# Performance work log

Hardware: AMD Instinct MI355X
Metric: run time of the kernel (lower is better)

The kernel has to match this reference:

```python
import jax, jax.numpy as jnp
import numpy as np

B, T, K, H = 8, 1024, 128, 8
TOP_K = 64
KS = 5  # conv kernel size for Q/K
DN = ('NCH', 'OIH', 'NCH')


def setup_inputs() -> dict:
    key = jax.random.key(0)
    ks = jax.random.split(key, 9)
    s = 0.05
    return {
        'x': jax.random.normal(ks[0], (B, T, K), jnp.float32),
        'Wq': jax.random.normal(ks[1], (K * H, K, KS), jnp.float32) * s,
        'bq': jax.random.normal(ks[2], (K * H,), jnp.float32) * s,
        'Wk': jax.random.normal(ks[3], (K * H, K, KS), jnp.float32) * s,
        'bk': jax.random.normal(ks[4], (K * H,), jnp.float32) * s,
        'Wv': jax.random.normal(ks[5], (K * H, K, 1), jnp.float32) * s,
        'bv': jax.random.normal(ks[6], (K * H,), jnp.float32) * s,
        'Wu': jax.random.normal(ks[7], (K, K * H), jnp.float32) * s,
        'bu': jax.random.normal(ks[8], (K,), jnp.float32) * s,
    }


def _prep(z, b, k, h, t, scale):
    # z: (b, k*h, t) conv output; torch view(b,k,h,t) then transposes -> (b,h,t,k)
    z = z.reshape(b, k, h, t)
    z = jnp.transpose(z, (0, 2, 3, 1)) * scale  # (b, h, t, k)
    # torch: transpose(1,2).contiguous().view(b*h, t, k) -- replicate exactly
    z = jnp.transpose(z, (0, 2, 1, 3)).reshape(b * h, t, k)
    return z


def reference(x, Wq, bq, Wk, bk, Wv, bv, Wu, bu):
    b, t, k = x.shape
    h = H
    xc = jnp.transpose(x, (0, 2, 1))  # (b, k, t)
    # causal left-pad KS-1 for Q/K convs; V is pointwise (kernel 1)
    q = jax.lax.conv_general_dilated(xc, Wq, (1,), [(KS - 1, 0)], dimension_numbers=DN) + bq[None, :, None]
    kk = jax.lax.conv_general_dilated(xc, Wk, (1,), [(KS - 1, 0)], dimension_numbers=DN) + bk[None, :, None]
    v = jax.lax.conv_general_dilated(xc, Wv, (1,), [(0, 0)], dimension_numbers=DN) + bv[None, :, None]
    scale = k ** -0.25
    q = _prep(q, b, k, h, t, scale)
    kk = _prep(kk, b, k, h, t, scale)
    v = _prep(v, b, k, h, t, 1.0)
    w = jnp.einsum('btk,bsk->bts', q, kk)  # (b*h, t, t)
    # top-k sparsification: keep entries >= k-th largest per row, else row min
    largest, _ = jax.lax.top_k(w, TOP_K)
    thresh = jnp.min(largest, axis=-1, keepdims=True)
    row_min = jnp.min(w, axis=-1, keepdims=True)
    w = jnp.where(w >= thresh, w, row_min)
    # causal mask (strict upper triangle -> -inf)
    causal = jnp.triu(jnp.ones((t, t), bool), 1)
    w = jnp.where(causal[None], -jnp.inf, w)
    w = jax.nn.softmax(w, axis=-1)
    out = jnp.einsum('bts,bsk->btk', w, v)  # (b*h, t, k)
    out = out.reshape(b, h, t, k)
    out = jnp.transpose(out, (0, 2, 1, 3)).reshape(b, t, k * h)
    return out @ Wu.T + bu
```

## Files before the change

### kernel.cpp

```cpp
#include <hip/hip_runtime.h>
#include <hip/hip_fp16.h>
#include <cstdint>

using f16 = _Float16;
typedef __attribute__((ext_vector_type(8))) _Float16 f16x8;
typedef __attribute__((ext_vector_type(4))) _Float16 f16x4;
typedef __attribute__((ext_vector_type(4))) float f32x4;

#define MFMA16(a, b, c) __builtin_amdgcn_mfma_f32_16x16x32_f16((a), (b), (c), 0, 0, 0)

__device__ __forceinline__ f16x8 ldfrag(const f16* p) { return *(const f16x8*)p; }

__device__ __forceinline__ void dma16(const f16* g, f16* l) {
  __builtin_amdgcn_global_load_lds(
      (const __attribute__((address_space(1))) void*)g,
      (__attribute__((address_space(3))) void*)l, 16, 0, 0);
}
__device__ __forceinline__ void wait_vm0() {
  asm volatile("s_waitcnt vmcnt(0)" ::: "memory");
}
__device__ __forceinline__ void wait_lgkm0() {
  asm volatile("s_waitcnt lgkmcnt(0)" ::: "memory");
}
__device__ __forceinline__ void wait_vm4() {
  asm volatile("s_waitcnt vmcnt(4)" ::: "memory");
}
__device__ __forceinline__ void wait_vm2() {
  asm volatile("s_waitcnt vmcnt(2)" ::: "memory");
}

static const int64_t NX = 1048576;
static const int64_t NW = 655360;
static const int64_t NV = 131072;

__global__ __launch_bounds__(256) void k0_prep(
    const float* __restrict__ x, const float* __restrict__ Wq,
    const float* __restrict__ Wk, const float* __restrict__ Wv,
    const float* __restrict__ Wu,
    f16* __restrict__ xh, f16* __restrict__ xl,
    f16* __restrict__ Wqh, f16* __restrict__ Wql,
    f16* __restrict__ Wkh, f16* __restrict__ Wkl,
    f16* __restrict__ Wvb, f16* __restrict__ Wub) {
  int64_t i = (int64_t)blockIdx.x * 256 + threadIdx.x;
  if (i < NX) {
    const float v = x[i];
    const f16 h = (f16)v;
    xh[i] = h; xl[i] = (f16)(v - (float)h);
  } else if (i < NX + NW) {
    int64_t d = i - NX;
    int j = (int)(d >> 17);
    int rem = (int)(d & 131071);
    int o = rem >> 7, c = rem & 127;
    const float v = Wq[(int64_t)(o * 128 + c) * 5 + j];
    const f16 h = (f16)v;
    Wqh[d] = h; Wql[d] = (f16)(v - (float)h);
  } else if (i < NX + 2 * NW) {
    int64_t d = i - NX - NW;
    int j = (int)(d >> 17);
    int rem = (int)(d & 131071);
    int o = rem >> 7, c = rem & 127;
    const float v = Wk[(int64_t)(o * 128 + c) * 5 + j];
    const f16 h = (f16)v;
    Wkh[d] = h; Wkl[d] = (f16)(v - (float)h);
  } else if (i < NX + 2 * NW + NV) {
    int64_t d = i - NX - 2 * NW;
    Wvb[d] = (f16)Wv[d];
  } else {
    int64_t d = i - NX - 2 * NW - NV;
    Wub[d] = (f16)Wu[d];
  }
}

#define STAGE_QK(DST, PASS, VALEXPR)                                    \
  {                                                                     \
    __syncthreads();                                                    \
    _Pragma("unroll")                                                   \
    for (int nt = 0; nt < 8; ++nt) {                                    \
      const int o = o0 + nt * 16 + lo;                                  \
      const int kcl = (o >> 3) & 63, hh = o & 7;                        \
      _Pragma("unroll")                                                 \
      for (int rtl = 0; rtl < 2; ++rtl) {                               \
        const int rt = (PASS) * 2 + rtl;                                \
        _Pragma("unroll")                                               \
        for (int r = 0; r < 4; ++r) {                                   \
          const int t2l = (rtl * 16 + quad * 4 + r) * 8 + hh;           \
          lds[t2l * 72 + kcl] = (VALEXPR);                              \
        }                                                               \
      }                                                                 \
    }                                                                   \
    __syncthreads();                                                    \
    _Pragma("unroll")                                                   \
    for (int p = 0; p < 8; ++p) {                                       \
      const int idx = p * 256 + tid;                                    \
      const int a = idx >> 3, c8 = (idx & 7) * 8;                       \
      *(f16x8*)(DST + ((int64_t)m * 1024 + t2b + (PASS) * 256 + a) * 128 + \
                half * 64 + c8) = *(const f16x8*)&lds[a * 72 + c8];     \
    }                                                                   \
  }

__global__ __launch_bounds__(256) void k1_conv(
    const f16* __restrict__ xh, const f16* __restrict__ xl,
    const f16* __restrict__ Wqh, const f16* __restrict__ Wql,
    const f16* __restrict__ Wkh, const f16* __restrict__ Wkl,
    const f16* __restrict__ Wvb,
    const float* __restrict__ bq, const float* __restrict__ bk,
    const float* __restrict__ bv,
    f16* __restrict__ q3h, f16* __restrict__ q3l,
    f16* __restrict__ k3h, f16* __restrict__ k3l,
    f16* __restrict__ v3T) {
  __shared__ f16 shm[36384];
  f16* const wbuf = shm;
  f16* const xbuf = shm + 18432;
  f16* const lds  = shm;
  const int tid = threadIdx.x;
  const int w = tid >> 6, lane = tid & 63;
  const int quad = lane >> 4, lo = lane & 15;
  const int r0 = blockIdx.x * 64;
  const int bb = r0 >> 10;
  const int m  = r0 >> 7;
  const int t2b = (r0 & 127) * 8;
  const int tloc = r0 & 1023;
  const int half = blockIdx.y;
  const int isK = blockIdx.z;
  const int o0 = half * 512 + w * 128;

  const f16* Wh = isK ? Wkh : Wqh;
  const f16* Wl = isK ? Wkl : Wql;
  const float* bias = isK ? bk : bq;

#pragma unroll
  for (int p = 0; p < 9; ++p) {
    const int u = p * 256 + tid;
    if (u < 2176) {
      const int row = u >> 5, tz = (u >> 4) & 1, c8 = (u & 15) * 8;
      int lt = tloc - 4 + row;
      if (lt < 0) lt = 0;
      const f16* src = (tz ? xl : xh) + ((int64_t)(bb * 1024 + lt)) * 128 + c8;
      *(f16x8*)&xbuf[row * 264 + tz * 128 + c8] = *(const f16x8*)src;
    }
  }
  __syncthreads();

  const int64_t wlane = (int64_t)(lane & 15) * 128 + (lane >> 4) * 8;

  if (!isK) {
    f32x4 av[4][8];
#pragma unroll
    for (int rt = 0; rt < 4; ++rt)
#pragma unroll
      for (int i = 0; i < 8; ++i)
#pragma unroll
        for (int r = 0; r < 4; ++r) av[rt][i][r] = 0.f;

#pragma unroll
    for (int g = 0; g < 4; ++g) {
#pragma unroll
      for (int s = 0; s < 2; ++s) {
        const int64_t vsrc = (int64_t)(o0 + (g * 2 + s) * 16) * 128 + wlane;
#pragma unroll
        for (int kk = 0; kk < 4; ++kk)
          dma16(Wvb + vsrc + kk * 32, wbuf + w * 4096 + s * 2048 + kk * 512);
      }
      wait_vm0();
#pragma unroll
      for (int kk = 0; kk < 4; ++kk) {
        f16x8 a[4];
#pragma unroll
        for (int rt = 0; rt < 4; ++rt)
          a[rt] = *(const f16x8*)&xbuf[(rt * 16 + lo + 4) * 264 + kk * 32 +
                                       quad * 8];
#pragma unroll
        for (int s = 0; s < 2; ++s) {
          const f16x8 bv8 = *(const f16x8*)&wbuf[w * 4096 + s * 2048 + kk * 512 +
                                                 quad * 128 + lo * 8];
#pragma unroll
          for (int rt = 0; rt < 4; ++rt)
            av[rt][g * 2 + s] = MFMA16(a[rt], bv8, av[rt][g * 2 + s]);
        }
      }
      wait_lgkm0();
    }
    __syncthreads();
#pragma unroll
    for (int pass = 0; pass < 2; ++pass) {
#pragma unroll
      for (int nt = 0; nt < 8; ++nt) {
        const int o = o0 + nt * 16 + lo;
        const float vbv = bv[o];
        const int kcl = (o >> 3) & 63, hh = o & 7;
#pragma unroll
        for (int rtl = 0; rtl < 2; ++rtl)
#pragma unroll
          for (int r = 0; r < 4; ++r) {
            const int t2l = (rtl * 16 + quad * 4 + r) * 8 + hh;
            lds[kcl * 264 + t2l] = (f16)(av[pass * 2 + rtl][nt][r] + vbv);
          }
      }
      __syncthreads();
#pragma unroll
      for (int p = 0; p < 8; ++p) {
        const int idx = p * 256 + tid;
        const int kcl = idx >> 5, t8 = (idx & 31) * 8;
        *(f16x8*)(v3T + ((int64_t)m * 128 + half * 64 + kcl) * 1024 + t2b +
                  pass * 256 + t8) = *(const f16x8*)&lds[kcl * 264 + t8];
      }
      __syncthreads();
    }
  }

  f32x4 aq[4][8];
#pragma unroll
  for (int rt = 0; rt < 4; ++rt)
#pragma unroll
    for (int i = 0; i < 8; ++i)
#pragma unroll
      for (int r = 0; r < 4; ++r) { aq[rt][i][r] = 0.f; }

  const int64_t wbase = wlane + (int64_t)o0 * 128;
#define ISSUE_HALF(J, KK, NTG, H)                                       \
  {                                                                     \
    _Pragma("unroll")                                                   \
    for (int ntl2 = 0; ntl2 < 2; ++ntl2) {                              \
      const int ntl_ = (H) * 2 + ntl2;                                  \
      const int64_t o_ = wbase + (int64_t)(J) * 131072 + (KK) * 32 +    \
                         (int64_t)(((NTG) * 4 + ntl_) * 16) * 128;      \
      dma16(Wh + o_, wbuf + w * 4096 + ntl_ * 1024);                    \
      dma16(Wl + o_, wbuf + w * 4096 + ntl_ * 1024 + 512);              \
    }                                                                   \
  }

  ISSUE_HALF(0, 0, 0, 0)
  ISSUE_HALF(0, 0, 0, 1)

  const bool z0 = (tloc == 0);
  for (int j = 0; j < 5; ++j) {
    f16x8 ah[4], al[4];
#pragma unroll
    for (int c = 0; c < 8; ++c) {
      const int kk = c >> 1, ntg = c & 1;
      if (ntg == 0) {
#pragma unroll
        for (int rt = 0; rt < 4; ++rt) {
          ah[rt] = *(const f16x8*)&xbuf[(rt * 16 + lo + j) * 264 + kk * 32 +
                                        quad * 8];
          al[rt] = *(const f16x8*)&xbuf[(rt * 16 + lo + j) * 264 + 128 +
                                        kk * 32 + quad * 8];
        }
        if (z0 && (lo + j < 4)) {
#pragma unroll
          for (int e = 0; e < 8; ++e) { ah[0][e] = (f16)0; al[0][e] = (f16)0; }
        }
      }
      const int nj = (c == 7) ? j + 1 : j;
      const int nkk = (c == 7) ? 0 : ((c + 1) >> 1);
      const int nntg = (c == 7) ? 0 : ((c + 1) & 1);
      const bool more = (c < 7) || (j < 4);

      wait_vm4();
#pragma unroll
      for (int ntl = 0; ntl < 2; ++ntl) {
        const int nt = ntg * 4 + ntl;
        const f16x8 bh = *(const f16x8*)&wbuf[w * 4096 + ntl * 1024 +
                                              quad * 128 + lo * 8];
        const f16x8 bl = *(const f16x8*)&wbuf[w * 4096 + ntl * 1024 + 512 +
                                              quad * 128 + lo * 8];
#pragma unroll
        for (int rt = 0; rt < 4; ++rt) {
          aq[rt][nt] = MFMA16(ah[rt], bh, aq[rt][nt]);
          aq[rt][nt] = MFMA16(ah[rt], bl, aq[rt][nt]);
          aq[rt][nt] = MFMA16(al[rt], bh, aq[rt][nt]);
        }
      }
      wait_lgkm0();
      if (more) ISSUE_HALF(nj, nkk, nntg, 0)

      if (c == 7) {
        if (j == 4) wait_vm0(); else wait_vm4();
      } else {
        wait_vm4();
      }
#pragma unroll
      for (int ntl = 2; ntl < 4; ++ntl) {
        const int nt = ntg * 4 + ntl;
        const f16x8 bh = *(const f16x8*)&wbuf[w * 4096 + ntl * 1024 +
                                              quad * 128 + lo * 8];
        const f16x8 bl = *(const f16x8*)&wbuf[w * 4096 + ntl * 1024 + 512 +
                                              quad * 128 + lo * 8];
#pragma unroll
        for (int rt = 0; rt < 4; ++rt) {
          aq[rt][nt] = MFMA16(ah[rt], bh, aq[rt][nt]);
          aq[rt][nt] = MFMA16(ah[rt], bl, aq[rt][nt]);
          aq[rt][nt] = MFMA16(al[rt], bh, aq[rt][nt]);
        }
      }
      wait_lgkm0();
      if (more) ISSUE_HALF(nj, nkk, nntg, 1)
    }
  }
#undef ISSUE_HALF

  const float SC = 0.29730177875068026f;
#pragma unroll
  for (int nt = 0; nt < 8; ++nt) {
    const int o = o0 + nt * 16 + lo;
    const float vb = bias[o];
#pragma unroll
    for (int rt = 0; rt < 4; ++rt)
#pragma unroll
      for (int r = 0; r < 4; ++r) aq[rt][nt][r] = (aq[rt][nt][r] + vb) * SC;
  }

  if (!isK) {
    STAGE_QK(q3h, 0, (f16)aq[rt][nt][r])
    STAGE_QK(q3h, 1, (f16)aq[rt][nt][r])
    STAGE_QK(q3l, 0, (f16)(aq[rt][nt][r] - (float)(f16)aq[rt][nt][r]))
    STAGE_QK(q3l, 1, (f16)(aq[rt][nt][r] - (float)(f16)aq[rt][nt][r]))
  } else {
    STAGE_QK(k3h, 0, (f16)aq[rt][nt][r])
    STAGE_QK(k3h, 1, (f16)aq[rt][nt][r])
    STAGE_QK(k3l, 0, (f16)(aq[rt][nt][r] - (float)(f16)aq[rt][nt][r]))
    STAGE_QK(k3l, 1, (f16)(aq[rt][nt][r] - (float)(f16)aq[rt][nt][r]))
  }
}

__global__ __launch_bounds__(512, 4) void k234_attn(
    const f16* __restrict__ q3h, const f16* __restrict__ q3l,
    const f16* __restrict__ k3h, const f16* __restrict__ k3l,
    const f16* __restrict__ v3T, f16* __restrict__ A) {
  __shared__ __align__(16) char smem[54016];
  float* const SbQ = (float*)smem;
  f16* const Pbuf = (f16*)smem;
  f16* const kbuf = (f16*)(smem + 17152);
  f16* const qlds = (f16*)(smem + 17152 + 32768);
  const int tid = threadIdx.x;
  const int w = tid >> 6, lane = tid & 63;
  const int quad = lane >> 4, lo = lane & 15;
  const int qd = lane & 3, cit = lane >> 2;
  const int qsw = qd ^ ((cit >> 1) & 3);
  const int fro = (lo * 4 + (quad ^ ((lo >> 1) & 3))) * 8;
  const int hid = blockIdx.y * 32 + blockIdx.x;
  const int m = (hid & 7) * 8 + ((hid >> 3) >> 5);
  const int r0 = ((hid >> 3) & 31) * 32;

  unsigned key[2][2][16];
  unsigned kmn[2][2];
#pragma unroll
  for (int g = 0; g < 2; ++g)
#pragma unroll
    for (int rr = 0; rr < 2; ++rr) kmn[g][rr] = 0xFFFFFFFFu;

#pragma unroll
  for (int half = 0; half < 2; ++half) {
    f32x4 acc[2][4];
#pragma unroll
    for (int g = 0; g < 2; ++g)
#pragma unroll
      for (int i = 0; i < 4; ++i)
#pragma unroll
        for (int r = 0; r < 4; ++r) acc[g][i][r] = 0.f;

    for (int kp = 0; kp < 2; ++kp) {
#pragma unroll
      for (int kkh = 0; kkh < 2; ++kkh) {
        __syncthreads();
        if (w < 4) {
          const int h_ = w & 1, grp_ = w >> 1;
          const f16* qsrc = (h_ ? q3l : q3h) +
              ((int64_t)m * 1024 + r0 + grp_ * 16 + lo) * 128 +
              (kp * 2 + kkh) * 32 + quad * 8;
          dma16(qsrc, qlds + w * 512);
        }
        wait_vm0();
        __syncthreads();

#define KISS(CC, PAIR)                                                   \
  {                                                                      \
    const int64_t rowg =                                                 \
        (int64_t)(m * 1024 + half * 512 + (CC) * 128 + w * 16 + cit) *   \
            128 + (kp * 2 + kkh) * 32 + qsw * 8;                         \
    dma16(k3h + rowg, kbuf + (w * 4 + (PAIR) * 2) * 512);                \
    dma16(k3l + rowg, kbuf + (w * 4 + (PAIR) * 2 + 1) * 512);            \
  }
        KISS(0, 0)
        KISS(1, 1)
#pragma unroll
        for (int cc = 0; cc < 4; ++cc) {
          if (cc < 3) wait_vm2();
          else wait_vm0();
          const int pair = cc & 1;
          const f16x8 qh0 = ldfrag(qlds + 0 * 512 + lane * 8);
          const f16x8 ql0 = ldfrag(qlds + 1 * 512 + lane * 8);
          const f16x8 qh1 = ldfrag(qlds + 2 * 512 + lane * 8);
          const f16x8 ql1 = ldfrag(qlds + 3 * 512 + lane * 8);
          const f16x8 bh =
              *(const f16x8*)(kbuf + (w * 4 + pair * 2) * 512 + fro);
          const f16x8 bl =
              *(const f16x8*)(kbuf + (w * 4 + pair * 2 + 1) * 512 + fro);
          acc[0][cc] = MFMA16(qh0, bh, acc[0][cc]);
          acc[0][cc] = MFMA16(qh0, bl, acc[0][cc]);
          acc[0][cc] = MFMA16(ql0, bh, acc[0][cc]);
          acc[1][cc] = MFMA16(qh1, bh, acc[1][cc]);
          acc[1][cc] = MFMA16(qh1, bl, acc[1][cc]);
          acc[1][cc] = MFMA16(ql1, bh, acc[1][cc]);
          wait_lgkm0();
          if (cc == 0) KISS(2, 0)
          if (cc == 1) KISS(3, 1)
        }
#undef KISS
      }
    }

#pragma unroll
    for (int grp = 0; grp < 2; ++grp) {
#pragma unroll
      for (int q = 0; q < 2; ++q) {
#pragma unroll
        for (int c2 = 0; c2 < 2; ++c2)
#pragma unroll
          for (int r = 0; r < 4; ++r)
            SbQ[(quad * 4 + r) * 268 + c2 * 128 + w * 16 + lo] =
                acc[grp][q * 2 + c2][r];
        __syncthreads();
#pragma unroll
        for (int rr = 0; rr < 2; ++rr) {
          const float4 f4 =
              *(const float4*)(SbQ + (w * 2 + rr) * 268 + lane * 4);
          const float fe[4] = {f4.x, f4.y, f4.z, f4.w};
#pragma unroll
          for (int e = 0; e < 4; ++e) {
            const unsigned u = __builtin_bit_cast(unsigned, fe[e]);
            const unsigned k = (u & 0x80000000u) ? ~u : (u | 0x80000000u);
            key[grp][rr][half * 8 + q * 4 + e] = k;
            kmn[grp][rr] = min(kmn[grp][rr], k);
          }
        }
        __syncthreads();
      }
    }
  }

  const int64_t vrow = (int64_t)(m * 128 + w * 16 + cit) * 1024;
#define VISSUE(KB, PAIR)                                                 \
  {                                                                      \
    dma16(v3T + vrow + (KB) * 64 + qsw * 8,                              \
          kbuf + (w * 4 + (PAIR) * 2) * 512);                            \
    dma16(v3T + vrow + (KB) * 64 + 32 + qsw * 8,                         \
          kbuf + (w * 4 + (PAIR) * 2 + 1) * 512);                        \
  }
  VISSUE(0, 0)
  if (r0 >= 64) VISSUE(1, 1)

#pragma unroll
  for (int off = 32; off; off >>= 1) {
#pragma unroll
    for (int g = 0; g < 2; ++g)
#pragma unroll
      for (int rr = 0; rr < 2; ++rr)
        kmn[g][rr] = min(kmn[g][rr],
                         (unsigned)__shfl_xor((int)kmn[g][rr], off));
  }
  unsigned th[2][2] = {{0u, 0u}, {0u, 0u}};
  {
    bool dn[2][2] = {{false, false}, {false, false}};
    for (int b = 31; b >= 0; --b) {
      bool all = true;
#pragma unroll
      for (int g = 0; g < 2; ++g)
#pragma unroll
        for (int rr = 0; rr < 2; ++rr) {
          if (!dn[g][rr]) {
            const unsigned c = th[g][rr] | (1u << b);
            int cnt = 0;
#pragma unroll
            for (int i = 0; i < 16; ++i)
              cnt += (int)__popcll(__ballot(key[g][rr][i] >= c));
            if (cnt >= 64) { th[g][rr] = c; if (cnt == 64) dn[g][rr] = true; }
          }
          all = all && dn[g][rr];
        }
      if (all) break;
    }
  }

#pragma unroll
  for (int grp = 0; grp < 2; ++grp) {
    const int nkb = ((r0 + grp * 16) >> 6) + 1;
    const int nkb0 = nkb < 8 ? nkb : 8;
    if (grp == 1) __syncthreads();

    float ev[2][16];
    float inv[2];
#pragma unroll
    for (int rr = 0; rr < 2; ++rr) {
      const unsigned kth = th[grp][rr];
      const unsigned kmv = kmn[grp][rr];
      const int t2 = r0 + grp * 16 + w * 2 + rr;
      const unsigned umn = (kmv & 0x80000000u) ? (kmv ^ 0x80000000u) : ~kmv;
      const float mn = __builtin_bit_cast(float, umn);
      const unsigned ukv = (kth & 0x80000000u) ? (kth ^ 0x80000000u) : ~kth;
      const float kv = __builtin_bit_cast(float, ukv);
      float sum = 0.f;
#pragma unroll
      for (int j = 0; j < 16; ++j) {
        const int s = (j >> 2) * 256 + lane * 4 + (j & 3);
        const unsigned k = key[grp][rr][j];
        const unsigned uu = (k & 0x80000000u) ? (k ^ 0x80000000u) : ~k;
        const float f = __builtin_bit_cast(float, uu);
        const float ww = (k >= kth) ? f : mn;
        const float x = (s <= t2) ? __expf(ww - kv) : 0.f;
        ev[rr][j] = x;
        sum += x;
      }
      for (int off = 32; off; off >>= 1) sum += __shfl_xor(sum, off);
      inv[rr] = 1.0f / sum;
    }

#pragma unroll
    for (int rr = 0; rr < 2; ++rr) {
      f16* prow = Pbuf + (w * 2 + rr) * 520;
#pragma unroll
      for (int i2 = 0; i2 < 2; ++i2) {
        f16x4 pk;
#pragma unroll
        for (int e = 0; e < 4; ++e)
          pk[e] = (f16)(ev[rr][i2 * 4 + e] * inv[rr]);
        *(f16x4*)(prow + i2 * 256 + lane * 4) = pk;
      }
    }
    __syncthreads();

    f32x4 oa0, oa1;
#pragma unroll
    for (int r = 0; r < 4; ++r) { oa0[r] = 0.f; oa1[r] = 0.f; }
    for (int kb = 0; kb < nkb0; ++kb) {
      if (kb + 1 < nkb0) wait_vm2();
      else wait_vm0();
      const int pair = kb & 1;
      {
        const f16x8 vf0 =
            *(const f16x8*)(kbuf + (w * 4 + pair * 2) * 512 + fro);
        const f16x8 vf1 =
            *(const f16x8*)(kbuf + (w * 4 + pair * 2 + 1) * 512 + fro);
        const f16x8 af0 = *(const f16x8*)(Pbuf + lo * 520 + kb * 64 + quad * 8);
        const f16x8 af1 =
            *(const f16x8*)(Pbuf + lo * 520 + kb * 64 + 32 + quad * 8);
        oa0 = MFMA16(af0, vf0, oa0);
        oa1 = MFMA16(af1, vf1, oa1);
      }
      wait_lgkm0();
      if (kb + 2 < nkb0) VISSUE(kb + 2, pair)
    }

    if (nkb > 8) {
      VISSUE(8, 0)
      if (nkb > 9) VISSUE(9, 1)
      __syncthreads();
#pragma unroll
      for (int rr = 0; rr < 2; ++rr) {
        f16* prow = Pbuf + (w * 2 + rr) * 520;
#pragma unroll
        for (int i2 = 0; i2 < 2; ++i2) {
          f16x4 pk;
#pragma unroll
          for (int e = 0; e < 4; ++e)
            pk[e] = (f16)(ev[rr][8 + i2 * 4 + e] * inv[rr]);
          *(f16x4*)(prow + i2 * 256 + lane * 4) = pk;
        }
      }
      __syncthreads();
      for (int kb = 8; kb < nkb; ++kb) {
        if (kb + 1 < nkb) wait_vm2();
        else wait_vm0();
        const int pair = kb & 1;
        {
          const f16x8 vf0 =
              *(const f16x8*)(kbuf + (w * 4 + pair * 2) * 512 + fro);
          const f16x8 vf1 =
              *(const f16x8*)(kbuf + (w * 4 + pair * 2 + 1) * 512 + fro);
          const f16x8 af0 =
              *(const f16x8*)(Pbuf + lo * 520 + (kb - 8) * 64 + quad * 8);
          const f16x8 af1 =
              *(const f16x8*)(Pbuf + lo * 520 + (kb - 8) * 64 + 32 + quad * 8);
          oa0 = MFMA16(af0, vf0, oa0);
          oa1 = MFMA16(af1, vf1, oa1);
        }
        wait_lgkm0();
        if (kb + 2 < nkb) VISSUE(kb + 2, pair)
      }
    }

    if (grp == 0) {
      VISSUE(0, 0)
      if (((r0 + 16) >> 6) + 1 > 1) VISSUE(1, 1)
    }
#pragma unroll
    for (int r = 0; r < 4; ++r)
      A[((int64_t)m * 1024 + r0 + grp * 16 + quad * 4 + r) * 128 + w * 16 +
        lo] = (f16)(oa0[r] + oa1[r]);
  }
#undef VISSUE
}

__global__ __launch_bounds__(256) void k5_proj(
    const f16* __restrict__ A, const f16* __restrict__ Wub,
    const float* __restrict__ bu, float* __restrict__ out) {
  const int w = threadIdx.x >> 6, lane = threadIdx.x & 63;
  const int quad = lane >> 4, lo = lane & 15;
  const int rt = w & 1, ch = w >> 1;
  const int r0 = blockIdx.x * 32 + rt * 16;
  const int r = r0 + lo;
  const int bI = r >> 10, t2 = r & 1023;

  f32x4 acc[4];
#pragma unroll
  for (int i = 0; i < 4; ++i)
#pragma unroll
    for (int rr = 0; rr < 4; ++rr) acc[i][rr] = 0.f;

#pragma unroll 2
  for (int kk = 0; kk < 32; ++kk) {
    const int o = kk * 32 + quad * 8;
    const int j = o >> 7, kc = o & 127;
    f16x8 a = ldfrag(A + (((int64_t)(bI * 8 + j) * 1024 + t2) * 128 + kc));
    f16x8 wb[4];
#pragma unroll
    for (int nt = 0; nt < 4; ++nt)
      wb[nt] = ldfrag(Wub + (int64_t)(ch * 64 + nt * 16 + lo) * 1024 + o);
#pragma unroll
    for (int nt = 0; nt < 4; ++nt) acc[nt] = MFMA16(a, wb[nt], acc[nt]);
  }
#pragma unroll
  for (int nt = 0; nt < 4; ++nt) {
    const int col = ch * 64 + nt * 16 + lo;
    const float bias = bu[col];
#pragma unroll
    for (int rr = 0; rr < 4; ++rr) {
      const int row = r0 + quad * 4 + rr;
      out[(int64_t)row * 128 + col] = acc[nt][rr] + bias;
    }
  }
}

extern "C" void kernel_launch(void* const* d_in, const int* in_sizes, int n_in,
                              void* d_out, int out_size, void* d_ws, size_t ws_size,
                              hipStream_t stream) {
  const float* x  = (const float*)d_in[0];
  const float* Wq = (const float*)d_in[1];
  const float* bq = (const float*)d_in[2];
  const float* Wk = (const float*)d_in[3];
  const float* bk = (const float*)d_in[4];
  const float* Wv = (const float*)d_in[5];
  const float* bv = (const float*)d_in[6];
  const float* Wu = (const float*)d_in[7];
  const float* bu = (const float*)d_in[8];
  float* out = (float*)d_out;

  char* ws = (char*)d_ws;
  f16* xh  = (f16*)ws;  ws += 2097152;
  f16* xl  = (f16*)ws;  ws += 2097152;
  f16* Wqh = (f16*)ws;  ws += 1310720;
  f16* Wql = (f16*)ws;  ws += 1310720;
  f16* Wkh = (f16*)ws;  ws += 1310720;
  f16* Wkl = (f16*)ws;  ws += 1310720;
  f16* Wvb = (f16*)ws;  ws += 262144;
  f16* Wub = (f16*)ws;  ws += 262144;
  f16* q3h = (f16*)ws;  ws += 16777216;
  f16* q3l = (f16*)ws;  ws += 16777216;
  f16* k3h = (f16*)ws;  ws += 16777216;
  f16* k3l = (f16*)ws;  ws += 16777216;
  f16* v3T = (f16*)ws;  ws += 16777216;
  f16* A   = (f16*)ws;  ws += 16777216;

  k0_prep<<<10240, 256, 0, stream>>>(x, Wq, Wk, Wv, Wu,
                                     xh, xl, Wqh, Wql, Wkh, Wkl, Wvb, Wub);

  k1_conv<<<dim3(128, 2, 2), 256, 0, stream>>>(xh, xl, Wqh, Wql, Wkh, Wkl, Wvb,
                                               bq, bk, bv, q3h, q3l, k3h, k3l,
                                               v3T);

  k234_attn<<<dim3(32, 64), 512, 0, stream>>>(q3h, q3l, k3h, k3l, v3T, A);

  k5_proj<<<256, 256, 0, stream>>>(A, Wub, bu, out);

  (void)in_sizes; (void)n_in; (void)out_size; (void)ws_size;
}
```

Baseline: 393.7 us.

## Merge two row-group PV passes into one pass sharing V tiles

The attention kernel used to run the P·V accumulation twice, once per 16-row group, and reloaded the V tiles by DMA for each. Now both groups' softmax probabilities are staged into two separate LDS buffers, and a single pass over V key blocks feeds four MFMAs per block. This halves the V global loads and removes one barrier-separated phase. In exchange, LDS use grows from about 54 KB to 70 KB per block and more registers are live, which may cut occupancy under launch_bounds(512,4). Group 0 now also iterates over group 1's extra key blocks, where its probabilities are zero.

```diff
diff --git a/kernel.cpp b/kernel.cpp
--- a/kernel.cpp
+++ b/kernel.cpp
@@ -327,11 +327,12 @@
     const f16* __restrict__ q3h, const f16* __restrict__ q3l,
     const f16* __restrict__ k3h, const f16* __restrict__ k3l,
     const f16* __restrict__ v3T, f16* __restrict__ A) {
-  __shared__ __align__(16) char smem[54016];
+  __shared__ __align__(16) char smem[70144];
   float* const SbQ = (float*)smem;
-  f16* const Pbuf = (f16*)smem;
-  f16* const kbuf = (f16*)(smem + 17152);
-  f16* const qlds = (f16*)(smem + 17152 + 32768);
+  f16* const PbufA = (f16*)smem;
+  f16* const PbufB = (f16*)(smem + 16640);
+  f16* const kbuf = (f16*)(smem + 33280);
+  f16* const qlds = (f16*)(smem + 66048);
   const int tid = threadIdx.x;
   const int w = tid >> 6, lane = tid & 63;
   const int quad = lane >> 4, lo = lane & 15;
@@ -440,15 +441,16 @@
   }
 
   const int64_t vrow = (int64_t)(m * 128 + w * 16 + cit) * 1024;
+  const int nkbM = ((r0 + 16) >> 6) + 1;
 #define VISSUE(KB, PAIR)                                                 \
   {                                                                      \
     dma16(v3T + vrow + (KB) * 64 + qsw * 8,                              \
           kbuf + (w * 4 + (PAIR) * 2) * 512);                            \
     dma16(v3T + vrow + (KB) * 64 + 32 + qsw * 8,                         \
-          kbuf + (w * 4 + (PAIR) * 2 + 1) * 512);                        \
+          kbuf + (w * 4 + (PAIR) * 2 + 1) * 512);                       \
   }
   VISSUE(0, 0)
-  if (r0 >= 64) VISSUE(1, 1)
+  if (nkbM > 1) VISSUE(1, 1)
 
 #pragma unroll
   for (int off = 32; off; off >>= 1) {
@@ -482,19 +484,15 @@
     }
   }
 
-#pragma unroll
-  for (int grp = 0; grp < 2; ++grp) {
-    const int nkb = ((r0 + grp * 16) >> 6) + 1;
-    const int nkb0 = nkb < 8 ? nkb : 8;
-    if (grp == 1) __syncthreads();
-
-    float ev[2][16];
-    float inv[2];
+  float ev[2][2][16];
+  float inv[2][2];
+#pragma unroll
+  for (int g = 0; g < 2; ++g)
 #pragma unroll
     for (int rr = 0; rr < 2; ++rr) {
-      const unsigned kth = th[grp][rr];
-      const unsigned kmv = kmn[grp][rr];
-      const int t2 = r0 + grp * 16 + w * 2 + rr;
+      const unsigned kth = th[g][rr];
+      const unsigned kmv = kmn[g][rr];
+      const int t2 = r0 + g * 16 + w * 2 + rr;
       const unsigned umn = (kmv & 0x80000000u) ? (kmv ^ 0x80000000u) : ~kmv;
       const float mn = __builtin_bit_cast(float, umn);
       const unsigned ukv = (kth & 0x80000000u) ? (kth ^ 0x80000000u) : ~kth;
@@ -503,37 +501,45 @@
 #pragma unroll
       for (int j = 0; j < 16; ++j) {
         const int s = (j >> 2) * 256 + lane * 4 + (j & 3);
-        const unsigned k = key[grp][rr][j];
+        const unsigned k = key[g][rr][j];
         const unsigned uu = (k & 0x80000000u) ? (k ^ 0x80000000u) : ~k;
         const float f = __builtin_bit_cast(float, uu);
         const float ww = (k >= kth) ? f : mn;
         const float x = (s <= t2) ? __expf(ww - kv) : 0.f;
-        ev[rr][j] = x;
+        ev[g][rr][j] = x;
         sum += x;
       }
       for (int off = 32; off; off >>= 1) sum += __shfl_xor(sum, off);
-      inv[rr] = 1.0f / sum;
-    }
-
-#pragma unroll
-    for (int rr = 0; rr < 2; ++rr) {
-      f16* prow = Pbuf + (w * 2 + rr) * 520;
-#pragma unroll
-      for (int i2 = 0; i2 < 2; ++i2) {
-        f16x4 pk;
-#pragma unroll
-        for (int e = 0; e < 4; ++e)
-          pk[e] = (f16)(ev[rr][i2 * 4 + e] * inv[rr]);
-        *(f16x4*)(prow + i2 * 256 + lane * 4) = pk;
+      inv[g][rr] = 1.0f / sum;
+    }
+
+  {
+    const int nkb0h = nkbM < 8 ? nkbM : 8;
+#pragma unroll
+    for (int g = 0; g < 2; ++g) {
+      f16* const pb = g ? PbufB : PbufA;
+#pragma unroll
+      for (int rr = 0; rr < 2; ++rr) {
+        f16* prow = pb + (w * 2 + rr) * 520;
+#pragma unroll
+        for (int i2 = 0; i2 < 2; ++i2) {
+          f16x4 pk;
+#pragma unroll
+          for (int e = 0; e < 4; ++e)
+            pk[e] = (f16)(ev[g][rr][i2 * 4 + e] * inv[g][rr]);
+          *(f16x4*)(prow + i2 * 256 + lane * 4) = pk;
+        }
       }
     }
     __syncthreads();
 
-    f32x4 oa0, oa1;
-#pragma unroll
-    for (int r = 0; r < 4; ++r) { oa0[r] = 0.f; oa1[r] = 0.f; }
-    for (int kb = 0; kb < nkb0; ++kb) {
-      if (kb + 1 < nkb0) wait_vm2();
+    f32x4 oaA0, oaA1, oaB0, oaB1;
+#pragma unroll
+    for (int r = 0; r < 4; ++r) {
+      oaA0[r] = 0.f; oaA1[r] = 0.f; oaB0[r] = 0.f; oaB1[r] = 0.f;
+    }
+    for (int kb = 0; kb < nkb0h; ++kb) {
+      if (kb + 1 < nkb0h) wait_vm2();
       else wait_vm0();
       const int pair = kb & 1;
       {
@@ -541,35 +547,46 @@
             *(const f16x8*)(kbuf + (w * 4 + pair * 2) * 512 + fro);
         const f16x8 vf1 =
             *(const f16x8*)(kbuf + (w * 4 + pair * 2 + 1) * 512 + fro);
-        const f16x8 af0 = *(const f16x8*)(Pbuf + lo * 520 + kb * 64 + quad * 8);
-        const f16x8 af1 =
-            *(const f16x8*)(Pbuf + lo * 520 + kb * 64 + 32 + quad * 8);
-        oa0 = MFMA16(af0, vf0, oa0);
-        oa1 = MFMA16(af1, vf1, oa1);
+        const f16x8 aA0 =
+            *(const f16x8*)(PbufA + lo * 520 + kb * 64 + quad * 8);
+        const f16x8 aA1 =
+            *(const f16x8*)(PbufA + lo * 520 + kb * 64 + 32 + quad * 8);
+        const f16x8 aB0 =
+            *(const f16x8*)(PbufB + lo * 520 + kb * 64 + quad * 8);
+        const f16x8 aB1 =
+            *(const f16x8*)(PbufB + lo * 520 + kb * 64 + 32 + quad * 8);
+        oaA0 = MFMA16(aA0, vf0, oaA0);
+        oaA1 = MFMA16(aA1, vf1, oaA1);
+        oaB0 = MFMA16(aB0, vf0, oaB0);
+        oaB1 = MFMA16(aB1, vf1, oaB1);
       }
       wait_lgkm0();
-      if (kb + 2 < nkb0) VISSUE(kb + 2, pair)
-    }
-
-    if (nkb > 8) {
+      if (kb + 2 < nkb0h) VISSUE(kb + 2, pair)
+    }
+
+    if (nkbM > 8) {
       VISSUE(8, 0)
-      if (nkb > 9) VISSUE(9, 1)
+      if (nkbM > 9) VISSUE(9, 1)
       __syncthreads();
 #pragma unroll
-      for (int rr = 0; rr < 2; ++rr) {
-        f16* prow = Pbuf + (w * 2 + rr) * 520;
-#pragma unroll
-        for (int i2 = 0; i2 < 2; ++i2) {
-          f16x4 pk;
-#pragma unroll
-          for (int e = 0; e < 4; ++e)
-            pk[e] = (f16)(ev[rr][8 + i2 * 4 + e] * inv[rr]);
-          *(f16x4*)(prow + i2 * 256 + lane * 4) = pk;
+      for (int g = 0; g < 2; ++g) {
+        f16* const pb = g ? PbufB : PbufA;
+#pragma unroll
+        for (int rr = 0; rr < 2; ++rr) {
+          f16* prow = pb + (w * 2 + rr) * 520;
+#pragma unroll
+          for (int i2 = 0; i2 < 2; ++i2) {
+            f16x4 pk;
+#pragma unroll
+            for (int e = 0; e < 4; ++e)
+              pk[e] = (f16)(ev[g][rr][8 + i2 * 4 + e] * inv[g][rr]);
+            *(f16x4*)(prow + i2 * 256 + lane * 4) = pk;
+          }
         }
       }
       __syncthreads();
-      for (int kb = 8; kb < nkb; ++kb) {
-        if (kb + 1 < nkb) wait_vm2();
+      for (int kb = 8; kb < nkbM; ++kb) {
+        if (kb + 1 < nkbM) wait_vm2();
         else wait_vm0();
         const int pair = kb & 1;
         {
@@ -577,26 +594,31 @@
               *(const f16x8*)(kbuf + (w * 4 + pair * 2) * 512 + fro);
           const f16x8 vf1 =
               *(const f16x8*)(kbuf + (w * 4 + pair * 2 + 1) * 512 + fro);
-          const f16x8 af0 =
-              *(const f16x8*)(Pbuf + lo * 520 + (kb - 8) * 64 + quad * 8);
-          const f16x8 af1 =
-              *(const f16x8*)(Pbuf + lo * 520 + (kb - 8) * 64 + 32 + quad * 8);
-          oa0 = MFMA16(af0, vf0, oa0);
-          oa1 = MFMA16(af1, vf1, oa1);
+          const f16x8 aA0 =
+              *(const f16x8*)(PbufA + lo * 520 + (kb - 8) * 64 + quad * 8);
+          const f16x8 aA1 =
+              *(const f16x8*)(PbufA + lo * 520 + (kb - 8) * 64 + 32 + quad * 8);
+          const f16x8 aB0 =
+              *(const f16x8*)(PbufB + lo * 520 + (kb - 8) * 64 + quad * 8);
+          const f16x8 aB1 =
+              *(const f16x8*)(PbufB + lo * 520 + (kb - 8) * 64 + 32 + quad * 8);
+          oaA0 = MFMA16(aA0, vf0, oaA0);
+          oaA1 = MFMA16(aA1, vf1, oaA1);
+          oaB0 = MFMA16(aB0, vf0, oaB0);
+          oaB1 = MFMA16(aB1, vf1, oaB1);
         }
         wait_lgkm0();
-        if (kb + 2 < nkb) VISSUE(kb + 2, pair)
-      }
-    }
-
-    if (grp == 0) {
-      VISSUE(0, 0)
-      if (((r0 + 16) >> 6) + 1 > 1) VISSUE(1, 1)
-    }
-#pragma unroll
-    for (int r = 0; r < 4; ++r)
-      A[((int64_t)m * 1024 + r0 + grp * 16 + quad * 4 + r) * 128 + w * 16 +
-        lo] = (f16)(oa0[r] + oa1[r]);
+        if (kb + 2 < nkbM) VISSUE(kb + 2, pair)
+      }
+    }
+
+#pragma unroll
+    for (int r = 0; r < 4; ++r) {
+      A[((int64_t)m * 1024 + r0 + quad * 4 + r) * 128 + w * 16 + lo] =
+          (f16)(oaA0[r] + oaA1[r]);
+      A[((int64_t)m * 1024 + r0 + 16 + quad * 4 + r) * 128 + w * 16 + lo] =
+          (f16)(oaB0[r] + oaB1[r]);
+    }
   }
 #undef VISSUE
 }
```

Measured after the change: 383.3 us. -2.7%, faster.
